# Kernel optimization log

Hardware: AMD Instinct MI355X
Metric: run time of the kernel (lower is better)

Reference implementation:

```python
import jax, jax.numpy as jnp
import numpy as np

LN_EPS = 1e-5


def _layer_norm(x, weight, bias):
    mean = jnp.mean(x, axis=-1, keepdims=True)
    var = jnp.var(x, axis=-1, keepdims=True)
    return (x - mean) * jax.lax.rsqrt(var + LN_EPS) * weight + bias


def _build_kernel(Lambda_real, Lambda_imag, C_real, C_imag, seq_length):
    # Lambda: [N] complex with negative real part -> stable decay
    lam = -jnp.exp(Lambda_real) + 1j * jnp.exp(Lambda_imag)
    C = (C_real + 1j * C_imag) * (jnp.exp(lam) - 1.0) / lam  # [H, N]
    t = jnp.arange(seq_length, dtype=Lambda_real.dtype)
    S = jnp.exp(lam[:, None] * t[None, :])  # [N, L] Vandermonde-like
    K = jnp.real(C @ S)  # [H, L]
    return K


def setup_inputs() -> dict:
    key = jax.random.key(0)
    ks = jax.random.split(key, 6)
    B, L, H, N = 8, 4096, 512, 512
    return {
        "x": jax.random.normal(ks[0], (B, L, H), dtype=jnp.float32),
        "ln_weight": jnp.ones((H,), dtype=jnp.float32),
        "ln_bias": jnp.zeros((H,), dtype=jnp.float32),
        "Lambda_real": jax.random.normal(ks[1], (N,), dtype=jnp.float32),
        "Lambda_imag": jax.random.normal(ks[2], (N,), dtype=jnp.float32),
        "C_real": jax.random.normal(ks[3], (H, N), dtype=jnp.float32),
        "C_imag": jax.random.normal(ks[4], (H, N), dtype=jnp.float32),
        "D": jax.random.normal(ks[5], (H,), dtype=jnp.float32),
    }


def reference(x, ln_weight, ln_bias, Lambda_real, Lambda_imag, C_real, C_imag, D):
    seq_length = x.shape[-2]
    K = _build_kernel(Lambda_real, Lambda_imag, C_real, C_imag, seq_length)  # [H, L]
    u = _layer_norm(x, ln_weight, ln_bias)  # [B, L, H]
    residual = u * D
    fft_length = 2 * seq_length
    u_f = jnp.fft.rfft(u, n=fft_length, axis=-2)          # [B, Lf, H] complex
    K_f = jnp.fft.rfft(K.T, n=fft_length, axis=-2)         # [Lf, H] complex
    y = jnp.fft.irfft(u_f * K_f, n=fft_length, axis=-2)[..., :seq_length, :]
    return y + residual
```

## Files before the change

kernel.cpp:

```cpp
#include <hip/hip_runtime.h>
#include <math.h>

#define BB 8
#define LL 4096
#define HH 512
#define NN 512
#define TT 192
#define NS 96
#define LT 16

typedef _Float16 half2_t __attribute__((ext_vector_type(2)));
typedef unsigned int u32;
typedef unsigned short u16;

#if __has_builtin(__builtin_amdgcn_fdot2)
__device__ __forceinline__ float fdot2(half2_t a, half2_t b, float c) {
    return __builtin_amdgcn_fdot2(a, b, c, false);
}
#else
__device__ __forceinline__ float fdot2(half2_t a, half2_t b, float c) {
    return c + (float)a.x * (float)b.x + (float)a.y * (float)b.y;
}
#endif

#define LN_BLKS (BB * LL / 8)
__global__ __launch_bounds__(256) void prep_kernel(const float* __restrict__ x,
                                                   const float* __restrict__ w,
                                                   const float* __restrict__ bia,
                                                   const float* __restrict__ Cr,
                                                   const float* __restrict__ Ci,
                                                   const float* __restrict__ LR,
                                                   const float* __restrict__ LI,
                                                   u32* __restrict__ u2,
                                                   float2* __restrict__ Cpk,
                                                   float2* __restrict__ PQ) {
    __shared__ float tile[64][65];
    if (blockIdx.x >= LN_BLKS + 64) {
        int n = blockIdx.x - (LN_BLKS + 64);
        int t = threadIdx.x;
        if (t < TT) {
            float lr = -expf(LR[n]);
            float li = expf(LI[n]);
            float el = expf(lr);
            float sn, cs;
            sincosf(li, &sn, &cs);
            float nr = el * cs - 1.0f;
            float ni = el * sn;
            float inv = 1.0f / (lr * lr + li * li);
            float sr = (nr * lr + ni * li) * inv;
            float si = (ni * lr - nr * li) * inv;
            float tf = (float)t;
            float e2 = expf(lr * tf);
            float s2, c2;
            sincosf(li * tf, &s2, &c2);
            float er = e2 * c2, ei = e2 * s2;
            PQ[(size_t)n * TT + t] = make_float2(sr * er - si * ei, sr * ei + si * er);
        }
        return;
    }
    if (blockIdx.x >= LN_BLKS) {
        int tb = blockIdx.x - LN_BLKS;
        int h0 = (tb & 7) * 64;
        int n0 = (tb >> 3) * 64;
        int c = threadIdx.x & 63;
        int r0 = threadIdx.x >> 6;
        float vr[16], vi[16];
        #pragma unroll
        for (int i = 0; i < 16; ++i) {
            int r = r0 + i * 4;
            tile[r][c] = Cr[(size_t)(h0 + r) * NN + n0 + c];
        }
        __syncthreads();
        #pragma unroll
        for (int i = 0; i < 16; ++i) vr[i] = tile[c][r0 + i * 4];
        __syncthreads();
        #pragma unroll
        for (int i = 0; i < 16; ++i) {
            int r = r0 + i * 4;
            tile[r][c] = Ci[(size_t)(h0 + r) * NN + n0 + c];
        }
        __syncthreads();
        #pragma unroll
        for (int i = 0; i < 16; ++i) vi[i] = tile[c][r0 + i * 4];
        #pragma unroll
        for (int i = 0; i < 16; ++i) {
            int r = r0 + i * 4;
            Cpk[(size_t)(n0 + r) * HH + h0 + c] = make_float2(vr[i], vi[i]);
        }
        return;
    }
    int wave = threadIdx.x >> 6;
    int lane = threadIdx.x & 63;
    size_t pair = (size_t)blockIdx.x * 4 + wave;
    const float* xr0 = x + pair * 2 * HH;
    const float* xr1 = xr0 + HH;
    float4 a0 = *(const float4*)(xr0 + lane * 4);
    float4 a1 = *(const float4*)(xr0 + 256 + lane * 4);
    float4 b0 = *(const float4*)(xr1 + lane * 4);
    float4 b1 = *(const float4*)(xr1 + 256 + lane * 4);
    float sA  = a0.x + a0.y + a0.z + a0.w + a1.x + a1.y + a1.z + a1.w;
    float qA  = a0.x*a0.x + a0.y*a0.y + a0.z*a0.z + a0.w*a0.w
              + a1.x*a1.x + a1.y*a1.y + a1.z*a1.z + a1.w*a1.w;
    float sB  = b0.x + b0.y + b0.z + b0.w + b1.x + b1.y + b1.z + b1.w;
    float qB  = b0.x*b0.x + b0.y*b0.y + b0.z*b0.z + b0.w*b0.w
              + b1.x*b1.x + b1.y*b1.y + b1.z*b1.z + b1.w*b1.w;
    #pragma unroll
    for (int off = 1; off < 64; off <<= 1) {
        sA += __shfl_xor(sA, off, 64);
        qA += __shfl_xor(qA, off, 64);
        sB += __shfl_xor(sB, off, 64);
        qB += __shfl_xor(qB, off, 64);
    }
    float mA = sA * (1.0f / 512.0f);
    float rA = rsqrtf(qA * (1.0f / 512.0f) - mA * mA + 1e-5f);
    float mB = sB * (1.0f / 512.0f);
    float rB = rsqrtf(qB * (1.0f / 512.0f) - mB * mB + 1e-5f);
    float4 w0 = *(const float4*)(w + lane * 4);
    float4 w1 = *(const float4*)(w + 256 + lane * 4);
    float4 c0 = *(const float4*)(bia + lane * 4);
    float4 c1 = *(const float4*)(bia + 256 + lane * 4);
    uint4 o0, o1;
    {
        half2_t p;
        p.x = (_Float16)((a0.x - mA) * rA * w0.x + c0.x);
        p.y = (_Float16)((b0.x - mB) * rB * w0.x + c0.x);
        o0.x = __builtin_bit_cast(u32, p);
        p.x = (_Float16)((a0.y - mA) * rA * w0.y + c0.y);
        p.y = (_Float16)((b0.y - mB) * rB * w0.y + c0.y);
        o0.y = __builtin_bit_cast(u32, p);
        p.x = (_Float16)((a0.z - mA) * rA * w0.z + c0.z);
        p.y = (_Float16)((b0.z - mB) * rB * w0.z + c0.z);
        o0.z = __builtin_bit_cast(u32, p);
        p.x = (_Float16)((a0.w - mA) * rA * w0.w + c0.w);
        p.y = (_Float16)((b0.w - mB) * rB * w0.w + c0.w);
        o0.w = __builtin_bit_cast(u32, p);
        p.x = (_Float16)((a1.x - mA) * rA * w1.x + c1.x);
        p.y = (_Float16)((b1.x - mB) * rB * w1.x + c1.x);
        o1.x = __builtin_bit_cast(u32, p);
        p.x = (_Float16)((a1.y - mA) * rA * w1.y + c1.y);
        p.y = (_Float16)((b1.y - mB) * rB * w1.y + c1.y);
        o1.y = __builtin_bit_cast(u32, p);
        p.x = (_Float16)((a1.z - mA) * rA * w1.z + c1.z);
        p.y = (_Float16)((b1.z - mB) * rB * w1.z + c1.z);
        o1.z = __builtin_bit_cast(u32, p);
        p.x = (_Float16)((a1.w - mA) * rA * w1.w + c1.w);
        p.y = (_Float16)((b1.w - mB) * rB * w1.w + c1.w);
        o1.w = __builtin_bit_cast(u32, p);
    }
    *(uint4*)(u2 + pair * HH + lane * 4) = o0;
    *(uint4*)(u2 + pair * HH + 256 + lane * 4) = o1;
}

__global__ __launch_bounds__(256) void build_kt(const float2* __restrict__ Cpk,
                                                const float2* __restrict__ PQ,
                                                float* __restrict__ KT) {
    int blk = blockIdx.x;
    int t0 = (blk >> 1) * 2;
    int half = blk & 1;
    int h = half * 256 + threadIdx.x;
    float k0 = 0.0f, k1 = 0.0f;
    const float4* pq4 = (const float4*)PQ;
    int pqoff = t0 >> 1;
    #pragma unroll 8
    for (int n = 0; n < NN; ++n) {
        float2 c = Cpk[(size_t)n * HH + h];
        float4 f = pq4[(size_t)n * (TT / 2) + pqoff];
        k0 = fmaf(c.x, f.x, k0);
        k0 = fmaf(-c.y, f.y, k0);
        k1 = fmaf(c.x, f.z, k1);
        k1 = fmaf(-c.y, f.w, k1);
    }
    KT[(size_t)t0 * HH + h] = k0;
    KT[(size_t)(t0 + 1) * HH + h] = k1;
}

__global__ void pack_k(const float* __restrict__ KT, uint2* __restrict__ KQ) {
    int idx = blockIdx.x * 256 + threadIdx.x;
    int s = idx >> 9;
    int h = idx & 511;
    float k0 = KT[(190 - 2 * s) * HH + h];
    float k1 = KT[(191 - 2 * s) * HH + h];
    float k2 = (s == 0) ? 0.0f : KT[(192 - 2 * s) * HH + h];
    half2_t kx, ky;
    kx.x = (_Float16)k1; kx.y = (_Float16)k0;
    ky.x = (_Float16)k2; ky.y = (_Float16)k1;
    KQ[idx] = make_uint2(__builtin_bit_cast(u32, kx), __builtin_bit_cast(u32, ky));
}


template <bool PRED>
__device__ __forceinline__ u32 load_v(const u32* __restrict__ ub2, int vi) {
    int c = vi;
    if (PRED && c < 0) c = 0;
    u32 val = ub2[(size_t)c * HH];
    if (PRED && vi < 0) val = 0u;
    return val;
}

#define SLOT(p) ((p) < 16 ? W[(p)] : X[(p) - 16])

template <bool PRED, bool LOADU>
__device__ __forceinline__ void conv_block(const u32* __restrict__ ub2,
                                           const uint2* klds,
                                           float (&acc)[LT], u32 (&W)[16], u32 (&X)[16],
                                           int ubase, int soff) {
    #pragma unroll
    for (int k = 0; k < 16; ++k) {
        u32 nv = 0u;
        if (LOADU) nv = load_v<PRED>(ub2, ubase + k);
        uint2 kq = klds[(soff + k) * 64];
        half2_t kx = __builtin_bit_cast(half2_t, kq.x);
        half2_t ky = __builtin_bit_cast(half2_t, kq.y);
        #pragma unroll
        for (int m = 0; m < 8; ++m) {
            half2_t ve = __builtin_bit_cast(half2_t, SLOT(k + m));
            half2_t vo = __builtin_bit_cast(half2_t, SLOT(k + m + 1));
            acc[2 * m]     = fdot2(ve, ky, acc[2 * m]);
            acc[2 * m + 1] = fdot2(vo, kx, acc[2 * m + 1]);
        }
        if (LOADU) W[k] = nv;
    }
}

template <bool PRED>
__device__ __forceinline__ void conv_all(const u32* __restrict__ ub2,
                                         const uint2* klds,
                                         float (&acc)[LT], u32 (&A)[16], u32 (&B)[16],
                                         int Vm1) {
    #pragma unroll
    for (int j = 0; j < 16; ++j) A[j] = load_v<PRED>(ub2, Vm1 + j);
    #pragma unroll
    for (int j = 0; j < 16; ++j) B[j] = load_v<PRED>(ub2, Vm1 + 16 + j);
    #pragma unroll 1
    for (int sbp = 0; sbp < 2; ++sbp) {
        conv_block<PRED, true>(ub2, klds, acc, A, B, Vm1 + 32 + 32 * sbp, 32 * sbp);
        conv_block<PRED, true>(ub2, klds, acc, B, A, Vm1 + 48 + 32 * sbp, 32 * sbp + 16);
    }
    conv_block<PRED, true>(ub2, klds, acc, A, B, Vm1 + 96, 64);
    conv_block<PRED, false>(ub2, klds, acc, B, A, 0, 80);
}

__global__ __launch_bounds__(512, 4) void conv_kernel(const u32* __restrict__ u2,
                                                      const uint2* __restrict__ KQ,
                                                      const float* __restrict__ KT,
                                                      const float* __restrict__ Dp,
                                                      float* __restrict__ y) {
    __shared__ uint2 KL[NS * 64];
    int tid = threadIdx.x;
    int lane = tid & 63;
    int g = tid >> 6;
    int blk = blockIdx.x;
    int hg = blk & 7;
    int tg = (blk >> 3) & 31;
    int b = blk >> 8;
    int h = hg * 64 + lane;
    int l0 = (tg * 8 + g) * LT;
    {
        const uint2* kg = KQ + hg * 64;
        #pragma unroll
        for (int it = 0; it < (NS * 64 / 2) / 512; ++it) {
            int i = it * 512 + tid;
            int s = i >> 5;
            int q = i & 31;
            uint4 v = *(const uint4*)(kg + (size_t)s * HH + q * 2);
            *(uint4*)(&KL[s * 64 + q * 2]) = v;
        }
    }
    __syncthreads();
    const u32* ub2 = u2 + (size_t)b * (LL / 2) * HH + h;
    const uint2* klds = &KL[lane];
    int Vm1 = l0 / 2 - NS;
    float acc[LT];
    u32 A[16], B[16];
    #pragma unroll
    for (int j = 0; j < LT; ++j) acc[j] = 0.0f;
    if (l0 >= TT) {
        conv_all<false>(ub2, klds, acc, A, B, Vm1);
    } else {
        conv_all<true>(ub2, klds, acc, A, B, Vm1);
    }
    float dv = Dp[h];
    float k0f = KT[h];
    float ce = k0f + dv;
    float* yb = y + ((size_t)b * LL + l0) * HH + h;
    #pragma unroll
    for (int m = 0; m < 8; ++m) {
        half2_t av = __builtin_bit_cast(half2_t, A[m]);
        float ue = (float)av.x;
        float uo = (float)av.y;
        yb[(size_t)(2 * m) * HH]     = acc[2 * m] + ce * ue;
        yb[(size_t)(2 * m + 1) * HH] = acc[2 * m + 1] + dv * uo;
    }
}

extern "C" void kernel_launch(void* const* d_in, const int* in_sizes, int n_in,
                              void* d_out, int out_size, void* d_ws, size_t ws_size,
                              hipStream_t stream) {
    const float* x   = (const float*)d_in[0];
    const float* lnw = (const float*)d_in[1];
    const float* lnb = (const float*)d_in[2];
    const float* LR  = (const float*)d_in[3];
    const float* LI  = (const float*)d_in[4];
    const float* Cr  = (const float*)d_in[5];
    const float* Ci  = (const float*)d_in[6];
    const float* Dp  = (const float*)d_in[7];
    float* y  = (float*)d_out;

    float2* Cpk = (float2*)d_ws;
    float2* PQ  = Cpk + (size_t)NN * HH;
    float*  KT  = (float*)(PQ + (size_t)NN * TT);
    uint2*  KQ  = (uint2*)(KT + (size_t)TT * HH);
    u32*    u2  = (u32*)(KQ + (size_t)NS * HH);

    prep_kernel<<<LN_BLKS + 64 + NN, 256, 0, stream>>>(x, lnw, lnb, Cr, Ci,
                                                       LR, LI, u2, Cpk, PQ);
    build_kt<<<TT, 256, 0, stream>>>(Cpk, PQ, KT);
    pack_k<<<NS * HH / 256, 256, 0, stream>>>(KT, KQ);
    conv_kernel<<<BB * (LL / (8 * LT)) * 8, 512, 0, stream>>>(u2, KQ, KT, Dp, y);
}
```

Baseline: 247.5 us.

## Halve per-thread output tile in conv and split build_kt reduction over two halves

The conv kernel now computes 8 outputs per thread instead of 16, using a single 24-entry rolling register window over all 96 taps. The grid doubles so each block covers half as many positions. This cuts register pressure and raises parallelism, but each thread now loads 100 u values for 8 outputs instead of 128 for 16, so global traffic per output goes up. Separately, build_kt uses 512 threads that split the N reduction in half and combine the two partial sums through shared memory, which shortens the serial loop.

New measurement: 219.4 us. -11.3%, faster.

```diff
diff --git a/kernel.cpp b/kernel.cpp
--- a/kernel.cpp
+++ b/kernel.cpp
@@ -7,7 +7,7 @@
 #define NN 512
 #define TT 192
 #define NS 96
-#define LT 16
+#define LT 8
 
 typedef _Float16 half2_t __attribute__((ext_vector_type(2)));
 typedef unsigned int u32;
@@ -151,18 +151,22 @@
     *(uint4*)(u2 + pair * HH + 256 + lane * 4) = o1;
 }
 
-__global__ __launch_bounds__(256) void build_kt(const float2* __restrict__ Cpk,
+__global__ __launch_bounds__(512) void build_kt(const float2* __restrict__ Cpk,
                                                 const float2* __restrict__ PQ,
                                                 float* __restrict__ KT) {
+    __shared__ float red[256][2];
     int blk = blockIdx.x;
     int t0 = (blk >> 1) * 2;
     int half = blk & 1;
-    int h = half * 256 + threadIdx.x;
+    int hh = threadIdx.x & 255;
+    int nh = threadIdx.x >> 8;
+    int h = half * 256 + hh;
     float k0 = 0.0f, k1 = 0.0f;
     const float4* pq4 = (const float4*)PQ;
     int pqoff = t0 >> 1;
+    int n0 = nh * 256;
     #pragma unroll 8
-    for (int n = 0; n < NN; ++n) {
+    for (int n = n0; n < n0 + 256; ++n) {
         float2 c = Cpk[(size_t)n * HH + h];
         float4 f = pq4[(size_t)n * (TT / 2) + pqoff];
         k0 = fmaf(c.x, f.x, k0);
@@ -170,8 +174,14 @@
         k1 = fmaf(c.x, f.z, k1);
         k1 = fmaf(-c.y, f.w, k1);
     }
-    KT[(size_t)t0 * HH + h] = k0;
-    KT[(size_t)(t0 + 1) * HH + h] = k1;
+    if (nh) { red[hh][0] = k0; red[hh][1] = k1; }
+    __syncthreads();
+    if (!nh) {
+        k0 += red[hh][0];
+        k1 += red[hh][1];
+        KT[(size_t)t0 * HH + h] = k0;
+        KT[(size_t)(t0 + 1) * HH + h] = k1;
+    }
 }
 
 __global__ void pack_k(const float* __restrict__ KT, uint2* __restrict__ KQ) {
@@ -197,47 +207,29 @@
     return val;
 }
 
-#define SLOT(p) ((p) < 16 ? W[(p)] : X[(p) - 16])
-
-template <bool PRED, bool LOADU>
-__device__ __forceinline__ void conv_block(const u32* __restrict__ ub2,
-                                           const uint2* klds,
-                                           float (&acc)[LT], u32 (&W)[16], u32 (&X)[16],
-                                           int ubase, int soff) {
-    #pragma unroll
-    for (int k = 0; k < 16; ++k) {
+template <bool PRED>
+__device__ __forceinline__ void conv96(const u32* __restrict__ ub2,
+                                       const uint2* klds,
+                                       float (&acc)[LT], u32 (&W)[24],
+                                       int Vm1) {
+    #pragma unroll
+    for (int i = 0; i < 24; ++i) W[i] = load_v<PRED>(ub2, Vm1 + i);
+    #pragma unroll
+    for (int s = 0; s < 96; ++s) {
         u32 nv = 0u;
-        if (LOADU) nv = load_v<PRED>(ub2, ubase + k);
-        uint2 kq = klds[(soff + k) * 64];
+        if (s < 76) nv = load_v<PRED>(ub2, Vm1 + s + 24);
+        uint2 kq = klds[s * 64];
         half2_t kx = __builtin_bit_cast(half2_t, kq.x);
         half2_t ky = __builtin_bit_cast(half2_t, kq.y);
         #pragma unroll
-        for (int m = 0; m < 8; ++m) {
-            half2_t ve = __builtin_bit_cast(half2_t, SLOT(k + m));
-            half2_t vo = __builtin_bit_cast(half2_t, SLOT(k + m + 1));
+        for (int m = 0; m < 4; ++m) {
+            half2_t ve = __builtin_bit_cast(half2_t, W[(s + m) % 24]);
+            half2_t vo = __builtin_bit_cast(half2_t, W[(s + m + 1) % 24]);
             acc[2 * m]     = fdot2(ve, ky, acc[2 * m]);
             acc[2 * m + 1] = fdot2(vo, kx, acc[2 * m + 1]);
         }
-        if (LOADU) W[k] = nv;
-    }
-}
-
-template <bool PRED>
-__device__ __forceinline__ void conv_all(const u32* __restrict__ ub2,
-                                         const uint2* klds,
-                                         float (&acc)[LT], u32 (&A)[16], u32 (&B)[16],
-                                         int Vm1) {
-    #pragma unroll
-    for (int j = 0; j < 16; ++j) A[j] = load_v<PRED>(ub2, Vm1 + j);
-    #pragma unroll
-    for (int j = 0; j < 16; ++j) B[j] = load_v<PRED>(ub2, Vm1 + 16 + j);
-    #pragma unroll 1
-    for (int sbp = 0; sbp < 2; ++sbp) {
-        conv_block<PRED, true>(ub2, klds, acc, A, B, Vm1 + 32 + 32 * sbp, 32 * sbp);
-        conv_block<PRED, true>(ub2, klds, acc, B, A, Vm1 + 48 + 32 * sbp, 32 * sbp + 16);
-    }
-    conv_block<PRED, true>(ub2, klds, acc, A, B, Vm1 + 96, 64);
-    conv_block<PRED, false>(ub2, klds, acc, B, A, 0, 80);
+        if (s < 76) W[s % 24] = nv;
+    }
 }
 
 __global__ __launch_bounds__(512, 4) void conv_kernel(const u32* __restrict__ u2,
@@ -251,8 +243,8 @@
     int g = tid >> 6;
     int blk = blockIdx.x;
     int hg = blk & 7;
-    int tg = (blk >> 3) & 31;
-    int b = blk >> 8;
+    int tg = (blk >> 3) & 63;
+    int b = blk >> 9;
     int h = hg * 64 + lane;
     int l0 = (tg * 8 + g) * LT;
     {
@@ -271,21 +263,21 @@
     const uint2* klds = &KL[lane];
     int Vm1 = l0 / 2 - NS;
     float acc[LT];
-    u32 A[16], B[16];
+    u32 W[24];
     #pragma unroll
     for (int j = 0; j < LT; ++j) acc[j] = 0.0f;
     if (l0 >= TT) {
-        conv_all<false>(ub2, klds, acc, A, B, Vm1);
+        conv96<false>(ub2, klds, acc, W, Vm1);
     } else {
-        conv_all<true>(ub2, klds, acc, A, B, Vm1);
+        conv96<true>(ub2, klds, acc, W, Vm1);
     }
     float dv = Dp[h];
     float k0f = KT[h];
     float ce = k0f + dv;
     float* yb = y + ((size_t)b * LL + l0) * HH + h;
     #pragma unroll
-    for (int m = 0; m < 8; ++m) {
-        half2_t av = __builtin_bit_cast(half2_t, A[m]);
+    for (int m = 0; m < 4; ++m) {
+        half2_t av = __builtin_bit_cast(half2_t, W[m]);
         float ue = (float)av.x;
         float uo = (float)av.y;
         yb[(size_t)(2 * m) * HH]     = acc[2 * m] + ce * ue;
@@ -314,7 +306,7 @@
 
     prep_kernel<<<LN_BLKS + 64 + NN, 256, 0, stream>>>(x, lnw, lnb, Cr, Ci,
                                                        LR, LI, u2, Cpk, PQ);
-    build_kt<<<TT, 256, 0, stream>>>(Cpk, PQ, KT);
+    build_kt<<<TT, 512, 0, stream>>>(Cpk, PQ, KT);
     pack_k<<<NS * HH / 256, 256, 0, stream>>>(KT, KQ);
     conv_kernel<<<BB * (LL / (8 * LT)) * 8, 512, 0, stream>>>(u2, KQ, KT, Dp, y);
 }
```
